# Performance work log

Hardware: AMD Instinct MI355X
Metric: run time of the kernel (lower is better)

## Reference

```python
import jax, jax.numpy as jnp
import numpy as np

B, S, E, H = 2, 2048, 1024, 16
D = E // H  # head_dim = 64


def setup_inputs() -> dict:
    key = jax.random.key(0)
    ks = jax.random.split(key, 11)
    s = 1.0 / np.sqrt(E)
    return {
        "query": jax.random.normal(ks[0], (B, S, E), jnp.float32),
        "key":   jax.random.normal(ks[1], (B, S, E), jnp.float32),
        "value": jax.random.normal(ks[2], (B, S, E), jnp.float32),
        "q_w": jax.random.uniform(ks[3], (E, E), jnp.float32, -s, s),
        "q_b": jax.random.uniform(ks[4], (E,), jnp.float32, -s, s),
        "k_w": jax.random.uniform(ks[5], (E, E), jnp.float32, -s, s),
        "k_b": jax.random.uniform(ks[6], (E,), jnp.float32, -s, s),
        "v_w": jax.random.uniform(ks[7], (E, E), jnp.float32, -s, s),
        "v_b": jax.random.uniform(ks[8], (E,), jnp.float32, -s, s),
        "o_w": jax.random.uniform(ks[9], (E, E), jnp.float32, -s, s),
        "o_b": jax.random.uniform(ks[10], (E,), jnp.float32, -s, s),
    }


def reference(query, key, value, q_w, q_b, k_w, k_b, v_w, v_b, o_w, o_b):
    b, sq, _ = query.shape
    sk = key.shape[1]
    # linear projections (torch Linear: x @ W.T + b)
    Q = (query @ q_w.T + q_b).reshape(b, sq, H, D).transpose(0, 2, 1, 3)  # b h sq d
    K = (key   @ k_w.T + k_b).reshape(b, sk, H, D).transpose(0, 2, 1, 3)
    V = (value @ v_w.T + v_b).reshape(b, sk, H, D).transpose(0, 2, 1, 3)
    scores = jnp.einsum("bhqd,bhkd->bhqk", Q, K) / jnp.sqrt(jnp.float32(D))
    attn = jax.nn.softmax(scores, axis=-1)
    out = jnp.einsum("bhqk,bhkd->bhqd", attn, V)  # b h sq d
    out = out.transpose(0, 2, 1, 3).reshape(b, sq, E)
    return out @ o_w.T + o_b
```

## Files before the change

kernel.cpp:

```cpp
#include <hip/hip_runtime.h>
#include <stdint.h>

typedef __bf16 bf16x8 __attribute__((ext_vector_type(8)));
typedef short short8 __attribute__((ext_vector_type(8)));
typedef float f32x4 __attribute__((ext_vector_type(4)));
typedef float f32x16 __attribute__((ext_vector_type(16)));
typedef unsigned short u16;
typedef unsigned int u32;

#define MROWS 4096
#define EDIM  1024
#define SQ    2048
#define DH    64

#if __has_builtin(__builtin_amdgcn_exp2f)
#define EXP2(x) __builtin_amdgcn_exp2f(x)
#else
#define EXP2(x) exp2f(x)
#endif

__device__ __forceinline__ u16 f2bf(float f) {
  unsigned u = __builtin_bit_cast(unsigned, f);
  return (u16)((u + 0x7FFFu + ((u >> 16) & 1u)) >> 16);
}

__device__ __forceinline__ u32 cvtpk_bf16(float lo, float hi) {
  u32 r;
  asm("v_cvt_pk_bf16_f32 %0, %1, %2" : "=v"(r) : "v"(lo), "v"(hi));
  return r;
}
__device__ __forceinline__ void swap32(u32& a, u32& b) {
  asm("v_permlane32_swap_b32 %0, %1" : "+v"(a), "+v"(b));
}

__global__ __launch_bounds__(256) void cvt_flat_kernel(
    const float* __restrict__ s0, const float* __restrict__ s1,
    const float* __restrict__ s2, const float* __restrict__ s3,
    const float* __restrict__ s4, const float* __restrict__ s5,
    const float* __restrict__ s6,
    u16* __restrict__ d0, u16* __restrict__ d1, u16* __restrict__ d2,
    u16* __restrict__ d3, u16* __restrict__ d4, u16* __restrict__ d5,
    u16* __restrict__ d6) {
  const int bid = blockIdx.x;
  const float* s; u16* d; int blk;
  if (bid < 6144) {
    const int t = bid >> 11;
    blk = bid & 2047;
    switch (t) {
      case 0: s = s0; d = d0; break;
      case 1: s = s1; d = d1; break;
      default: s = s2; d = d2; break;
    }
  } else {
    const int t = (bid - 6144) >> 9;
    blk = (bid - 6144) & 511;
    switch (t) {
      case 0: s = s3; d = d3; break;
      case 1: s = s4; d = d4; break;
      case 2: s = s5; d = d5; break;
      default: s = s6; d = d6; break;
    }
  }
  const int i = (blk * 256 + threadIdx.x) * 8;
  float4 a = *(const float4*)(s + i);
  float4 b = *(const float4*)(s + i + 4);
  short8 r;
  r[0] = (short)f2bf(a.x); r[1] = (short)f2bf(a.y);
  r[2] = (short)f2bf(a.z); r[3] = (short)f2bf(a.w);
  r[4] = (short)f2bf(b.x); r[5] = (short)f2bf(b.y);
  r[6] = (short)f2bf(b.z); r[7] = (short)f2bf(b.w);
  *(short8*)(d + i) = r;
}

template <int OUT_F32>
__device__ __forceinline__ void gemm_core(
    const u16* __restrict__ A, const u16* __restrict__ W,
    const float* __restrict__ bias, void* __restrict__ C,
    int m0, int n0, u16* As, u16* Bs) {
  const int tid = threadIdx.x, lane = tid & 63, w = tid >> 6;
  const int r = lane & 15, g = lane >> 4;
  const int wr = w >> 1, wc = w & 1;
  f32x4 acc[4][4] = {};

  for (int kt = 0; kt < 32; ++kt) {
    const int k0 = kt * 32;
    __syncthreads();
#pragma unroll
    for (int i = 0; i < 2; ++i) {
      int c = i * 256 + tid;
      int row = c >> 2, ko = (c & 3) * 8;
      __builtin_amdgcn_global_load_lds(
          (const __attribute__((address_space(1))) void*)(A + (size_t)(m0 + row) * EDIM + k0 + ko),
          (__attribute__((address_space(3))) void*)(As + (i * 256 + w * 64) * 8), 16, 0, 0);
      __builtin_amdgcn_global_load_lds(
          (const __attribute__((address_space(1))) void*)(W + (size_t)(n0 + row) * EDIM + k0 + ko),
          (__attribute__((address_space(3))) void*)(Bs + (i * 256 + w * 64) * 8), 16, 0, 0);
    }
    __syncthreads();
    bf16x8 af[4], bfv[4];
#pragma unroll
    for (int i = 0; i < 4; ++i) {
      af[i]  = *(const bf16x8*)&As[(wr * 64 + i * 16 + r) * 32 + g * 8];
      bfv[i] = *(const bf16x8*)&Bs[(wc * 64 + i * 16 + r) * 32 + g * 8];
    }
#pragma unroll
    for (int mi = 0; mi < 4; ++mi)
#pragma unroll
      for (int ni = 0; ni < 4; ++ni)
        acc[mi][ni] = __builtin_amdgcn_mfma_f32_16x16x32_bf16(af[mi], bfv[ni], acc[mi][ni], 0, 0, 0);
  }
#pragma unroll
  for (int ni = 0; ni < 4; ++ni) {
    const int col = n0 + wc * 64 + ni * 16 + r;
    const float bv = bias[col];
#pragma unroll
    for (int mi = 0; mi < 4; ++mi) {
#pragma unroll
      for (int rr = 0; rr < 4; ++rr) {
        const int rowm = m0 + wr * 64 + mi * 16 + g * 4 + rr;
        float v = acc[mi][ni][rr] + bv;
        if (OUT_F32) ((float*)C)[(size_t)rowm * EDIM + col] = v;
        else ((u16*)C)[(size_t)rowm * EDIM + col] = f2bf(v);
      }
    }
  }
}

__global__ __launch_bounds__(256) void gemm_qkv(
    const u16* __restrict__ X0, const u16* __restrict__ X1, const u16* __restrict__ X2,
    const u16* __restrict__ W0, const u16* __restrict__ W1, const u16* __restrict__ W2,
    const float* __restrict__ b0, const float* __restrict__ b1, const float* __restrict__ b2,
    u16* __restrict__ C0, u16* __restrict__ C1, u16* __restrict__ C2) {
  __shared__ u16 As[128 * 32];
  __shared__ u16 Bs[128 * 32];
  const u16 *A, *W; const float* bias; u16* C;
  switch (blockIdx.z) {
    case 0: A = X0; W = W0; bias = b0; C = C0; break;
    case 1: A = X1; W = W1; bias = b1; C = C1; break;
    default: A = X2; W = W2; bias = b2; C = C2; break;
  }
  gemm_core<0>(A, W, bias, C, blockIdx.y * 128, blockIdx.x * 128, As, Bs);
}

__global__ __launch_bounds__(256) void gemm_oproj(
    const u16* __restrict__ A, const u16* __restrict__ W,
    const float* __restrict__ bias, float* __restrict__ C) {
  __shared__ __align__(16) u16 As[128 * 32];
  __shared__ __align__(16) u16 Bs[64 * 32];
  const int tid = threadIdx.x, lane = tid & 63, w = tid >> 6;
  const int r = lane & 15, g = lane >> 4;
  const int m0 = blockIdx.y * 128, n0 = blockIdx.x * 64;
  const int wr = w >> 1, wc = w & 1;
  f32x4 acc[4][2] = {};

  for (int kt = 0; kt < 32; ++kt) {
    const int k0 = kt * 32;
    __syncthreads();
#pragma unroll
    for (int i = 0; i < 2; ++i) {
      const int c = i * 256 + tid;
      const int row = c >> 2, ko = (c & 3) * 8;
      __builtin_amdgcn_global_load_lds(
          (const __attribute__((address_space(1))) void*)(A + (size_t)(m0 + row) * EDIM + k0 + ko),
          (__attribute__((address_space(3))) void*)(As + (i * 256 + w * 64) * 8), 16, 0, 0);
    }
    {
      const int c = tid;
      const int row = c >> 2, ko = (c & 3) * 8;
      __builtin_amdgcn_global_load_lds(
          (const __attribute__((address_space(1))) void*)(W + (size_t)(n0 + row) * EDIM + k0 + ko),
          (__attribute__((address_space(3))) void*)(Bs + (w * 64) * 8), 16, 0, 0);
    }
    __syncthreads();
    bf16x8 af[4], bfv[2];
#pragma unroll
    for (int i = 0; i < 4; ++i)
      af[i] = *(const bf16x8*)&As[(wr * 64 + i * 16 + r) * 32 + g * 8];
#pragma unroll
    for (int i = 0; i < 2; ++i)
      bfv[i] = *(const bf16x8*)&Bs[(wc * 32 + i * 16 + r) * 32 + g * 8];
#pragma unroll
    for (int mi = 0; mi < 4; ++mi)
#pragma unroll
      for (int ni = 0; ni < 2; ++ni)
        acc[mi][ni] = __builtin_amdgcn_mfma_f32_16x16x32_bf16(af[mi], bfv[ni], acc[mi][ni], 0, 0, 0);
  }
#pragma unroll
  for (int ni = 0; ni < 2; ++ni) {
    const int col = n0 + wc * 32 + ni * 16 + r;
    const float bv = bias[col];
#pragma unroll
    for (int mi = 0; mi < 4; ++mi)
#pragma unroll
      for (int rr = 0; rr < 4; ++rr) {
        const int rowm = m0 + wr * 64 + mi * 16 + g * 4 + rr;
        C[(size_t)rowm * EDIM + col] = acc[mi][ni][rr] + bv;
      }
  }
}

__device__ __forceinline__ void k_stage(const u16* __restrict__ Kg, int kt, int tid,
                                        int w, u16* kb) {
#pragma unroll
  for (int ri = 0; ri < 2; ++ri) {
    int idx = ri * 256 + tid, row = idx >> 3, sl = idx & 7;
    __builtin_amdgcn_global_load_lds(
        (const __attribute__((address_space(1))) void*)(
            Kg + (size_t)(kt * 64 + row) * EDIM + ((sl ^ (row & 7)) * 8)),
        (__attribute__((address_space(3))) void*)(kb + (ri * 256 + w * 64) * 8), 16, 0, 0);
  }
}

__device__ __forceinline__ void v_issue(const u16* __restrict__ Vg, int kt, int tid,
                                        u32* vdw) {
  const int vd0 = (tid & 31) * 2, kvc = tid >> 5;
#pragma unroll
  for (int j = 0; j < 8; ++j)
    vdw[j] = *(const u32*)(Vg + (size_t)(kt * 64 + kvc * 8 + j) * EDIM + vd0);
}

__device__ __forceinline__ void v_write(u16* vt, int tid, const u32* vdw) {
  const int vd0 = (tid & 31) * 2, kvc = tid >> 5;
  union { u32 u[4]; short8 s; } lo8, hi8;
#pragma unroll
  for (int i = 0; i < 4; ++i) {
    lo8.u[i] = (vdw[2 * i] & 0xFFFFu) | (vdw[2 * i + 1] << 16);
    hi8.u[i] = (vdw[2 * i] >> 16) | (vdw[2 * i + 1] & 0xFFFF0000u);
  }
  const int sl = kvc ^ (vd0 & 7);
  *(short8*)&vt[vd0 * 64 + sl * 8] = lo8.s;
  *(short8*)&vt[(vd0 + 1) * 64 + (sl ^ 1) * 8] = hi8.s;
}

#define CE_CONST 0.18033688011112042f

__device__ __forceinline__ void qk_step(f32x16 (&st)[2], const u16* kb,
                                        const bf16x8 (&qf)[4], const int (&colA)[4],
                                        int lq) {
  __builtin_amdgcn_s_setprio(1);
#pragma unroll
  for (int t = 0; t < 2; ++t) {
    f32x16 z = {};
#pragma unroll
    for (int f = 0; f < 4; ++f) {
      const bf16x8 ka = *(const bf16x8*)&kb[(t * 32 + lq) * 64 + colA[f]];
      z = __builtin_amdgcn_mfma_f32_32x32x16_bf16(ka, qf[f], z, 0, 0, 0);
    }
    st[t] = z;
  }
  __builtin_amdgcn_s_setprio(0);
}

__device__ __forceinline__ void softmax_pb(f32x16 (&st)[2], float& m, float& l,
                                           f32x16 (&accO)[2], bf16x8 (&pb)[4]) {
  float vm = fmaxf(st[0][0], st[0][1]);
#pragma unroll
  for (int t = 0; t < 2; ++t)
#pragma unroll
    for (int rr = (t == 0 ? 2 : 0); rr < 16; ++rr) vm = fmaxf(vm, st[t][rr]);
  vm = fmaxf(vm, __shfl_xor(vm, 32));
  if (!__all(vm <= m + 8.0f)) {
    const float mn = fmaxf(m, vm);
    const float scl = EXP2((m - mn) * CE_CONST);
    m = mn;
    l *= scl;
#pragma unroll
    for (int dt = 0; dt < 2; ++dt)
#pragma unroll
      for (int rr = 0; rr < 16; ++rr) accO[dt][rr] *= scl;
  }
  const float mc = m * CE_CONST;
  float ts = 0.f;
#pragma unroll
  for (int t = 0; t < 2; ++t)
#pragma unroll
    for (int rr = 0; rr < 16; ++rr) {
      float pv = EXP2(st[t][rr] * CE_CONST - mc);
      st[t][rr] = pv;
      ts += pv;
    }
  ts += __shfl_xor(ts, 32);
  l += ts;
#pragma unroll
  for (int t = 0; t < 2; ++t)
#pragma unroll
    for (int kh = 0; kh < 2; ++kh) {
      const int rb = kh * 8;
      u32 a0 = cvtpk_bf16(st[t][rb + 0], st[t][rb + 1]);
      u32 b0 = cvtpk_bf16(st[t][rb + 4], st[t][rb + 5]);
      swap32(a0, b0);
      u32 a1 = cvtpk_bf16(st[t][rb + 2], st[t][rb + 3]);
      u32 b1 = cvtpk_bf16(st[t][rb + 6], st[t][rb + 7]);
      swap32(a1, b1);
      union { u32 u[4]; bf16x8 v; } pu;
      pu.u[0] = a0; pu.u[1] = a1; pu.u[2] = b0; pu.u[3] = b1;
      pb[t * 2 + kh] = pu.v;
    }
}

__device__ __forceinline__ void pv_step(f32x16 (&accO)[2], const bf16x8 (&pb)[4],
                                        const u16* vt, const int (&colA)[4], int lq) {
  __builtin_amdgcn_s_setprio(1);
#pragma unroll
  for (int dt = 0; dt < 2; ++dt)
#pragma unroll
    for (int ks = 0; ks < 4; ++ks) {
      const bf16x8 va = *(const bf16x8*)&vt[(dt * 32 + lq) * 64 + colA[ks]];
      accO[dt] = __builtin_amdgcn_mfma_f32_32x32x16_bf16(va, pb[ks], accO[dt], 0, 0, 0);
    }
  __builtin_amdgcn_s_setprio(0);
}

__global__ __launch_bounds__(256) void attn2_kernel(
    const u16* __restrict__ Q, const u16* __restrict__ K,
    const u16* __restrict__ V, u16* __restrict__ O) {
  __shared__ __align__(16) u16 KB[2][64 * 64];
  __shared__ __align__(16) u16 VT[3][64 * 64];
  const int tid = threadIdx.x, lane = tid & 63, w = tid >> 6;
  const int lq = lane & 31, hi = lane >> 5;
  const int bid = blockIdx.x;
  const int b2 = (bid & 7) * 64 + (bid >> 3);
  const int qb = b2 & 15, bh = b2 >> 4;
  const int b = bh >> 4, h = bh & 15;
  const u16* Qg = Q + (size_t)b * SQ * EDIM + h * DH;
  const u16* Kg = K + (size_t)b * SQ * EDIM + h * DH;
  const u16* Vg = V + (size_t)b * SQ * EDIM + h * DH;
  const int q0 = qb * 128 + w * 32;

  bf16x8 qf[4];
#pragma unroll
  for (int f = 0; f < 4; ++f)
    qf[f] = *(const bf16x8*)(Qg + (size_t)(q0 + lq) * EDIM + f * 16 + hi * 8);

  const int swz = (lq & 7) << 4;
  int colA[4];
#pragma unroll
  for (int f = 0; f < 4; ++f) colA[f] = ((f * 32 + hi * 16) ^ swz) >> 1;

  f32x16 accO[2] = {};
  f32x16 stA[2], stB[2];
  bf16x8 pb[4];
  float m = -3e38f, l = 0.f;
  u32 vdw[8];

  k_stage(Kg, 0, tid, w, KB[0]);
  v_issue(Vg, 0, tid, vdw);
  v_write(VT[0], tid, vdw);
  __syncthreads();
  k_stage(Kg, 1, tid, w, KB[1]);
  v_issue(Vg, 1, tid, vdw);
  qk_step(stA, KB[0], qf, colA, lq);
  v_write(VT[1], tid, vdw);
  __syncthreads();

#define ATTN_BODY(T, SP, SN)                                                  \
  {                                                                           \
    if ((T) < 31) { k_stage(Kg, (T) + 1, tid, w, KB[((T) + 1) & 1]);          \
                    v_issue(Vg, (T) + 1, tid, vdw); }                         \
    qk_step(SN, KB[(T) & 1], qf, colA, lq);                                   \
    softmax_pb(SP, m, l, accO, pb);                                           \
    pv_step(accO, pb, VT[((T) - 1) % 3], colA, lq);                           \
    if ((T) < 31) v_write(VT[((T) + 1) % 3], tid, vdw);                       \
    __syncthreads();                                                          \
  }

  for (int t = 1; t < 31; t += 2) {
    ATTN_BODY(t, stA, stB);
    ATTN_BODY(t + 1, stB, stA);
  }
  ATTN_BODY(31, stA, stB);
#undef ATTN_BODY

  softmax_pb(stB, m, l, accO, pb);
  pv_step(accO, pb, VT[31 % 3], colA, lq);

  const float rinv = 1.0f / l;
  u16* Ost = (u16*)KB;
#pragma unroll
  for (int dt = 0; dt < 2; ++dt)
#pragma unroll
    for (int rr = 0; rr < 16; ++rr) {
      const int d = dt * 32 + (rr & 3) + 8 * (rr >> 2) + 4 * hi;
      Ost[w * 2048 + lq * 64 + (d ^ ((lq & 7) << 3))] = f2bf(accO[dt][rr] * rinv);
    }
  __syncthreads();
#pragma unroll
  for (int ri = 0; ri < 4; ++ri) {
    const int idx = ri * 256 + tid;
    const int w2 = idx >> 8, q = (idx >> 3) & 31, c = idx & 7;
    short8 o = *(const short8*)&Ost[w2 * 2048 + q * 64 + ((c ^ (q & 7)) * 8)];
    *(short8*)(O + (size_t)(b * SQ + qb * 128 + w2 * 32 + q) * EDIM + h * DH + c * 8) = o;
  }
}

extern "C" void kernel_launch(void* const* d_in, const int* in_sizes, int n_in,
                              void* d_out, int out_size, void* d_ws, size_t ws_size,
                              hipStream_t stream) {
  (void)in_sizes; (void)n_in; (void)out_size; (void)ws_size;
  const float* query = (const float*)d_in[0];
  const float* key   = (const float*)d_in[1];
  const float* value = (const float*)d_in[2];
  const float* q_w = (const float*)d_in[3];
  const float* q_b = (const float*)d_in[4];
  const float* k_w = (const float*)d_in[5];
  const float* k_b = (const float*)d_in[6];
  const float* v_w = (const float*)d_in[7];
  const float* v_b = (const float*)d_in[8];
  const float* o_w = (const float*)d_in[9];
  const float* o_b = (const float*)d_in[10];

  u16* ws = (u16*)d_ws;
  const size_t NX = (size_t)MROWS * EDIM;
  const size_t NW = (size_t)EDIM * EDIM;
  u16* Xq = ws;
  u16* Xk = Xq + NX;
  u16* Xv = Xk + NX;
  u16* Wq = Xv + NX;
  u16* Wk = Wq + NW;
  u16* Wv = Wk + NW;
  u16* Wo = Wv + NW;
  u16* Qp = Wo + NW;
  u16* Kp = Qp + NX;
  u16* Vp = Kp + NX;
  u16* At = Xq;

  cvt_flat_kernel<<<8192, 256, 0, stream>>>(
      query, key, value, q_w, k_w, v_w, o_w,
      Xq, Xk, Xv, Wq, Wk, Wv, Wo);

  gemm_qkv<<<dim3(8, 32, 3), 256, 0, stream>>>(
      Xq, Xk, Xv, Wq, Wk, Wv, q_b, k_b, v_b, Qp, Kp, Vp);

  attn2_kernel<<<512, 256, 0, stream>>>(Qp, Kp, Vp, At);

  gemm_oproj<<<dim3(16, 32), 256, 0, stream>>>(At, Wo, o_b, (float*)d_out);
}
```

Baseline: 135.1 us.

## Split attention KV range across two wave groups and merge softmax partials

The attention kernel now launches 512 threads per block: two groups of four waves each process half of the key/value sequence for the same 128 query rows. The two partial softmax states are merged through LDS before normalisation. This doubles the waves working per block, aiming to raise latency hiding and occupancy. In exchange it drops the software pipelining of QK against softmax/PV, adds merge traffic and syncs, and uses more LDS per block.

```diff
diff --git a/kernel.cpp b/kernel.cpp
--- a/kernel.cpp
+++ b/kernel.cpp
@@ -199,28 +199,28 @@
   }
 }
 
-__device__ __forceinline__ void k_stage(const u16* __restrict__ Kg, int kt, int tid,
-                                        int w, u16* kb) {
+__device__ __forceinline__ void k_stage(const u16* __restrict__ Kg, int kt, int lt,
+                                        int lw, u16* kb) {
 #pragma unroll
   for (int ri = 0; ri < 2; ++ri) {
-    int idx = ri * 256 + tid, row = idx >> 3, sl = idx & 7;
+    int idx = ri * 256 + lt, row = idx >> 3, sl = idx & 7;
     __builtin_amdgcn_global_load_lds(
         (const __attribute__((address_space(1))) void*)(
             Kg + (size_t)(kt * 64 + row) * EDIM + ((sl ^ (row & 7)) * 8)),
-        (__attribute__((address_space(3))) void*)(kb + (ri * 256 + w * 64) * 8), 16, 0, 0);
-  }
-}
-
-__device__ __forceinline__ void v_issue(const u16* __restrict__ Vg, int kt, int tid,
+        (__attribute__((address_space(3))) void*)(kb + (ri * 256 + lw * 64) * 8), 16, 0, 0);
+  }
+}
+
+__device__ __forceinline__ void v_issue(const u16* __restrict__ Vg, int kt, int lt,
                                         u32* vdw) {
-  const int vd0 = (tid & 31) * 2, kvc = tid >> 5;
+  const int vd0 = (lt & 31) * 2, kvc = lt >> 5;
 #pragma unroll
   for (int j = 0; j < 8; ++j)
     vdw[j] = *(const u32*)(Vg + (size_t)(kt * 64 + kvc * 8 + j) * EDIM + vd0);
 }
 
-__device__ __forceinline__ void v_write(u16* vt, int tid, const u32* vdw) {
-  const int vd0 = (tid & 31) * 2, kvc = tid >> 5;
+__device__ __forceinline__ void v_write(u16* vt, int lt, const u32* vdw) {
+  const int vd0 = (lt & 31) * 2, kvc = lt >> 5;
   union { u32 u[4]; short8 s; } lo8, hi8;
 #pragma unroll
   for (int i = 0; i < 4; ++i) {
@@ -311,21 +311,22 @@
   __builtin_amdgcn_s_setprio(0);
 }
 
-__global__ __launch_bounds__(256) void attn2_kernel(
+__global__ __launch_bounds__(512) void attn3_kernel(
     const u16* __restrict__ Q, const u16* __restrict__ K,
     const u16* __restrict__ V, u16* __restrict__ O) {
-  __shared__ __align__(16) u16 KB[2][64 * 64];
-  __shared__ __align__(16) u16 VT[3][64 * 64];
+  __shared__ __align__(16) u16 KB[2][2][64 * 64];
+  __shared__ __align__(16) u16 VT[2][2][64 * 64];
   const int tid = threadIdx.x, lane = tid & 63, w = tid >> 6;
+  const int sp = w >> 2, qw = w & 3, lt = tid & 255;
   const int lq = lane & 31, hi = lane >> 5;
   const int bid = blockIdx.x;
   const int b2 = (bid & 7) * 64 + (bid >> 3);
   const int qb = b2 & 15, bh = b2 >> 4;
   const int b = bh >> 4, h = bh & 15;
   const u16* Qg = Q + (size_t)b * SQ * EDIM + h * DH;
-  const u16* Kg = K + (size_t)b * SQ * EDIM + h * DH;
-  const u16* Vg = V + (size_t)b * SQ * EDIM + h * DH;
-  const int q0 = qb * 128 + w * 32;
+  const u16* Kg = K + (size_t)b * SQ * EDIM + h * DH + (size_t)sp * 1024 * EDIM;
+  const u16* Vg = V + (size_t)b * SQ * EDIM + h * DH + (size_t)sp * 1024 * EDIM;
+  const int q0 = qb * 128 + qw * 32;
 
   bf16x8 qf[4];
 #pragma unroll
@@ -338,55 +339,77 @@
   for (int f = 0; f < 4; ++f) colA[f] = ((f * 32 + hi * 16) ^ swz) >> 1;
 
   f32x16 accO[2] = {};
-  f32x16 stA[2], stB[2];
+  f32x16 st[2];
   bf16x8 pb[4];
   float m = -3e38f, l = 0.f;
   u32 vdw[8];
 
-  k_stage(Kg, 0, tid, w, KB[0]);
-  v_issue(Vg, 0, tid, vdw);
-  v_write(VT[0], tid, vdw);
+  k_stage(Kg, 0, lt, qw, KB[sp][0]);
+  v_issue(Vg, 0, lt, vdw);
+  v_write(VT[sp][0], lt, vdw);
   __syncthreads();
-  k_stage(Kg, 1, tid, w, KB[1]);
-  v_issue(Vg, 1, tid, vdw);
-  qk_step(stA, KB[0], qf, colA, lq);
-  v_write(VT[1], tid, vdw);
+
+  for (int T = 0; T < 16; ++T) {
+    if (T < 15) {
+      k_stage(Kg, T + 1, lt, qw, KB[sp][(T + 1) & 1]);
+      v_issue(Vg, T + 1, lt, vdw);
+    }
+    qk_step(st, KB[sp][T & 1], qf, colA, lq);
+    softmax_pb(st, m, l, accO, pb);
+    pv_step(accO, pb, VT[sp][T & 1], colA, lq);
+    if (T < 15) v_write(VT[sp][(T + 1) & 1], lt, vdw);
+    __syncthreads();
+  }
+
+  float* mrgf = (float*)&KB[0][0][0];
+  float* sttf = (float*)&VT[0][0][0];
+  if (sp == 1) {
+#pragma unroll
+    for (int dt = 0; dt < 2; ++dt)
+#pragma unroll
+      for (int rr = 0; rr < 16; ++rr) {
+        const int d = dt * 32 + (rr & 3) + 8 * (rr >> 2) + 4 * hi;
+        mrgf[(qw * 32 + lq) * 64 + ((d + 2 * lq) & 63)] = accO[dt][rr];
+      }
+    if (lane < 32) {
+      sttf[(qw * 32 + lq) * 2 + 0] = m;
+      sttf[(qw * 32 + lq) * 2 + 1] = l;
+    }
+  }
   __syncthreads();
-
-#define ATTN_BODY(T, SP, SN)                                                  \
-  {                                                                           \
-    if ((T) < 31) { k_stage(Kg, (T) + 1, tid, w, KB[((T) + 1) & 1]);          \
-                    v_issue(Vg, (T) + 1, tid, vdw); }                         \
-    qk_step(SN, KB[(T) & 1], qf, colA, lq);                                   \
-    softmax_pb(SP, m, l, accO, pb);                                           \
-    pv_step(accO, pb, VT[((T) - 1) % 3], colA, lq);                           \
-    if ((T) < 31) v_write(VT[((T) + 1) % 3], tid, vdw);                       \
-    __syncthreads();                                                          \
-  }
-
-  for (int t = 1; t < 31; t += 2) {
-    ATTN_BODY(t, stA, stB);
-    ATTN_BODY(t + 1, stB, stA);
-  }
-  ATTN_BODY(31, stA, stB);
-#undef ATTN_BODY
-
-  softmax_pb(stB, m, l, accO, pb);
-  pv_step(accO, pb, VT[31 % 3], colA, lq);
-
-  const float rinv = 1.0f / l;
+  if (sp == 0) {
+    const float m1 = sttf[(qw * 32 + lq) * 2 + 0];
+    const float l1 = sttf[(qw * 32 + lq) * 2 + 1];
+    const float ms = fmaxf(m, m1);
+    const float e0 = EXP2((m - ms) * CE_CONST);
+    const float e1 = EXP2((m1 - ms) * CE_CONST);
+    l = l * e0 + l1 * e1;
+#pragma unroll
+    for (int dt = 0; dt < 2; ++dt)
+#pragma unroll
+      for (int rr = 0; rr < 16; ++rr) {
+        const int d = dt * 32 + (rr & 3) + 8 * (rr >> 2) + 4 * hi;
+        accO[dt][rr] = accO[dt][rr] * e0 +
+                       mrgf[(qw * 32 + lq) * 64 + ((d + 2 * lq) & 63)] * e1;
+      }
+  }
+  __syncthreads();
+
   u16* Ost = (u16*)KB;
-#pragma unroll
-  for (int dt = 0; dt < 2; ++dt)
-#pragma unroll
-    for (int rr = 0; rr < 16; ++rr) {
-      const int d = dt * 32 + (rr & 3) + 8 * (rr >> 2) + 4 * hi;
-      Ost[w * 2048 + lq * 64 + (d ^ ((lq & 7) << 3))] = f2bf(accO[dt][rr] * rinv);
-    }
+  if (sp == 0) {
+    const float rinv = 1.0f / l;
+#pragma unroll
+    for (int dt = 0; dt < 2; ++dt)
+#pragma unroll
+      for (int rr = 0; rr < 16; ++rr) {
+        const int d = dt * 32 + (rr & 3) + 8 * (rr >> 2) + 4 * hi;
+        Ost[qw * 2048 + lq * 64 + (d ^ ((lq & 7) << 3))] = f2bf(accO[dt][rr] * rinv);
+      }
+  }
   __syncthreads();
 #pragma unroll
-  for (int ri = 0; ri < 4; ++ri) {
-    const int idx = ri * 256 + tid;
+  for (int ri = 0; ri < 2; ++ri) {
+    const int idx = ri * 512 + tid;
     const int w2 = idx >> 8, q = (idx >> 3) & 31, c = idx & 7;
     short8 o = *(const short8*)&Ost[w2 * 2048 + q * 64 + ((c ^ (q & 7)) * 8)];
     *(short8*)(O + (size_t)(b * SQ + qb * 128 + w2 * 32 + q) * EDIM + h * DH + c * 8) = o;
@@ -431,7 +454,7 @@
   gemm_qkv<<<dim3(8, 32, 3), 256, 0, stream>>>(
       Xq, Xk, Xv, Wq, Wk, Wv, q_b, k_b, v_b, Qp, Kp, Vp);
 
-  attn2_kernel<<<512, 256, 0, stream>>>(Qp, Kp, Vp, At);
+  attn3_kernel<<<512, 512, 0, stream>>>(Qp, Kp, Vp, At);
 
   gemm_oproj<<<dim3(16, 32), 256, 0, stream>>>(At, Wo, o_b, (float*)d_out);
 }
```

After: 127.7 us, median of 3. 5.5% less time.
